# Kernel optimization log

Hardware: AMD Instinct MI355X
Metric: run time of the kernel (lower is better)

## Reference

```python
import jax, jax.numpy as jnp
import numpy as np

# ---- static config (aegnn GraphRes, ncars, spline convs) ----
B, NPG, DEG = 16, 6400, 8            # graphs per batch, nodes per graph, avg degree
N = B * NPG                          # 102400 nodes
E = N * DEG                          # 819200 edges
W_IMG, H_IMG = 120, 100              # input_shape[:2]
PSX, PSY = 16, 12                    # pooling_size
GX, GY = 8, 9                        # ceil(120/16), ceil(100/12)
G = GX * GY                          # 72 voxel-grid cells per graph
CH = [1, 8, 16, 16, 16, 32, 32, 32]  # n[] channel ladder, conv1..conv7
KK = 8                               # kernel_size**dim = 2**3 spline kernels
NUM_OUT = 2


def setup_inputs() -> dict:
    key = jax.random.key(0)
    ks = jax.random.split(key, 16)
    x = jax.random.normal(ks[0], (N, 1), jnp.float32)
    # event positions: (x,y,t) with x in [0,120), y in [0,100), t in [0,1)
    pos = jax.random.uniform(ks[1], (N, 3), jnp.float32) * jnp.array([W_IMG, H_IMG, 1.0], jnp.float32)
    # within-graph random edges
    eg = jax.random.randint(ks[2], (E,), 0, B)
    src = eg * NPG + jax.random.randint(ks[3], (E,), 0, NPG)
    dst = eg * NPG + jax.random.randint(ks[4], (E,), 0, NPG)
    edge_index = jnp.stack([src, dst]).astype(jnp.int32)
    # pseudo-coordinates (normalized relative positions) in [0,1]^3
    edge_attr = jax.random.uniform(ks[5], (E, 3), jnp.float32)
    batch = (jnp.arange(N) // NPG).astype(jnp.int32)
    params = {}
    for i in range(7):
        cin, cout = CH[i], CH[i + 1]
        params[f"w{i+1}"] = jax.random.normal(ks[6 + i], (KK, cin, cout), jnp.float32) / np.float32(np.sqrt(cin * KK))
    fc_w = jax.random.normal(ks[13], (G * CH[-1], NUM_OUT), jnp.float32) * 0.02
    return dict(x=x, pos=pos, edge_attr=edge_attr, edge_index=edge_index, batch=batch,
                fc_w=fc_w, **params)


def _spline_basis(edge_attr):
    """Degree-1 open B-spline basis, kernel_size=2 per dim -> dense [E, 8].
    With K=2: v = u*(K-1) = u, so per-dim basis is [1-u, u].
    Flattened kernel index = k0 + 2*k1 + 4*k2 (dim0 fastest, as in torch_spline_conv)."""
    u = jnp.clip(edge_attr, 0.0, 1.0)
    b = jnp.stack([1.0 - u, u], axis=-1)                      # [E, 3, 2]
    full = jnp.einsum('ea,eb,ec->ecba', b[:, 0], b[:, 1], b[:, 2])  # [E, k2, k1, k0]
    return full.reshape(-1, KK)


def _spline_conv(x, src, dst, basis, Wk):
    """SplineConv(bias=False, root_weight=False, aggr='mean')."""
    xj = x[src]                                               # gather [E, Cin]
    out = basis[:, 0:1] * (xj @ Wk[0])
    for k in range(1, KK):                                    # fixed 8 kernels
        out = out + basis[:, k:k + 1] * (xj @ Wk[k])
    agg = jax.ops.segment_sum(out, dst, num_segments=N)
    cnt = jax.ops.segment_sum(jnp.ones((src.shape[0], 1), x.dtype), dst, num_segments=N)
    return agg / jnp.maximum(cnt, 1.0)


def reference(x, pos, edge_attr, edge_index, batch, fc_w, w1, w2, w3, w4, w5, w6, w7):
    src, dst = edge_index[0], edge_index[1]
    basis = _spline_basis(edge_attr)                          # [E, 8]
    act = jax.nn.elu
    h = act(_spline_conv(x, src, dst, basis, w1))             # 1 -> 8
    h = act(_spline_conv(h, src, dst, basis, w2))             # 8 -> 16
    h_sc = h
    h = act(_spline_conv(h, src, dst, basis, w3))             # 16 -> 16
    h = act(_spline_conv(h, src, dst, basis, w4))             # 16 -> 16
    h = h + h_sc                                              # residual
    h = act(_spline_conv(h, src, dst, basis, w5))             # 16 -> 32
    h_sc = h
    h = act(_spline_conv(h, src, dst, basis, w6))             # 32 -> 32
    h = act(_spline_conv(h, src, dst, basis, w7))             # 32 -> 32
    h = h + h_sc                                              # residual
    # voxel-grid max pooling over (x, y) with cell size pooling_size
    cx = jnp.floor(pos[:, 0] / PSX).astype(jnp.int32)
    cy = jnp.floor(pos[:, 1] / PSY).astype(jnp.int32)
    cluster = batch * G + cy * GX + cx                        # [N]
    pooled = jax.ops.segment_max(h, cluster, num_segments=B * G)
    pooled = jnp.where(jnp.isfinite(pooled), pooled, 0.0)     # empty cells -> 0
    return pooled.reshape(B, G * CH[-1]) @ fc_w               # [B, num_outputs]
```

## Files before the change

kernel.cpp:

```cpp
#include <hip/hip_runtime.h>
#include <math.h>

namespace {
constexpr int N  = 102400;
constexpr int E  = 819200;
constexpr int B_ = 16;
constexpr int G  = 72;
constexpr int GX = 8;
constexpr int NB = N / 256;
constexpr int EB = E / 256;
}


__global__ __launch_bounds__(256) void count_kernel(const int* __restrict__ ei,
                                                    int* __restrict__ cnt) {
  int e = blockIdx.x * 256 + threadIdx.x;
  atomicAdd(&cnt[ei[E + e]], 1);
}

__global__ __launch_bounds__(256) void rcnt_kernel(const int* __restrict__ cnt,
                                                   float* __restrict__ rcnt) {
  int n = blockIdx.x * 256 + threadIdx.x;
  rcnt[n] = 1.0f / (float)max(cnt[n], 1);
}

__global__ __launch_bounds__(256) void reduce_cnt(const int* __restrict__ cnt,
                                                  int* __restrict__ bsum) {
  __shared__ int s[256];
  int i = blockIdx.x * 256 + threadIdx.x;
  s[threadIdx.x] = cnt[i];
  __syncthreads();
  for (int st = 128; st > 0; st >>= 1) {
    if (threadIdx.x < st) s[threadIdx.x] += s[threadIdx.x + st];
    __syncthreads();
  }
  if (threadIdx.x == 0) bsum[blockIdx.x] = s[0];
}

__global__ __launch_bounds__(512) void scan_bsum(const int* __restrict__ bsum,
                                                 int* __restrict__ boff) {
  __shared__ int s[512];
  int i = threadIdx.x;
  int v = (i < NB) ? bsum[i] : 0;
  s[i] = v;
  __syncthreads();
  for (int st = 1; st < 512; st <<= 1) {
    int t = (i >= st) ? s[i - st] : 0;
    __syncthreads();
    s[i] += t;
    __syncthreads();
  }
  if (i < NB) boff[i] = s[i] - v;
}

__global__ __launch_bounds__(256) void write_rowptr(const int* __restrict__ cnt,
                                                    const int* __restrict__ boff,
                                                    int* __restrict__ rowptr,
                                                    int* __restrict__ cursor) {
  __shared__ int s[256];
  int i = blockIdx.x * 256 + threadIdx.x;
  int v = cnt[i];
  s[threadIdx.x] = v;
  __syncthreads();
  for (int st = 1; st < 256; st <<= 1) {
    int t = (threadIdx.x >= st) ? s[threadIdx.x - st] : 0;
    __syncthreads();
    s[threadIdx.x] += t;
    __syncthreads();
  }
  int off = boff[blockIdx.x] + s[threadIdx.x] - v;
  rowptr[i] = off;
  cursor[i] = off;
  if (i == N - 1) rowptr[N] = off + v;
}

__global__ __launch_bounds__(256) void edge_scatter(const int* __restrict__ ei,
                                                    const float* __restrict__ ea,
                                                    int* __restrict__ cursor,
                                                    float4* __restrict__ rec) {
  int e = blockIdx.x * 256 + threadIdx.x;
  int src = ei[e];
  int dst = ei[E + e];
  float u0 = fminf(fmaxf(ea[3 * e + 0], 0.f), 1.f);
  float u1 = fminf(fmaxf(ea[3 * e + 1], 0.f), 1.f);
  float u2 = fminf(fmaxf(ea[3 * e + 2], 0.f), 1.f);
  int slot = atomicAdd(&cursor[dst], 1);
  rec[slot] = make_float4(__int_as_float(src), u0, u1, u2);
}


__global__ __launch_bounds__(256) void block_hist(const int* __restrict__ cnt,
                                                  int* __restrict__ bh) {
  __shared__ int h[64];
  if (threadIdx.x < 64) h[threadIdx.x] = 0;
  __syncthreads();
  int n = blockIdx.x * 256 + threadIdx.x;
  atomicAdd(&h[min(cnt[n], 63)], 1);
  __syncthreads();
  if (threadIdx.x < 64) bh[threadIdx.x * NB + blockIdx.x] = h[threadIdx.x];
}

__global__ __launch_bounds__(256) void scan_bh(int* __restrict__ bh) {
  constexpr int TOT = 64 * NB;
  constexpr int CH  = TOT / 256;
  __shared__ int part[256];
  const int t = threadIdx.x;
  const int base = t * CH;
  int s = 0;
  for (int i = 0; i < CH; i++) s += bh[base + i];
  part[t] = s;
  __syncthreads();
  for (int st = 1; st < 256; st <<= 1) {
    int v = (t >= st) ? part[t - st] : 0;
    __syncthreads();
    part[t] += v;
    __syncthreads();
  }
  int run = part[t] - s;
  for (int i = 0; i < CH; i++) {
    int v = bh[base + i];
    bh[base + i] = run;
    run += v;
  }
}

__global__ __launch_bounds__(256) void order_block(const int* __restrict__ cnt,
                                                   const int* __restrict__ bh,
                                                   const int* __restrict__ rowptr,
                                                   int* __restrict__ order,
                                                   int2* __restrict__ sdesc) {
  __shared__ int cur[64];
  if (threadIdx.x < 64) cur[threadIdx.x] = 0;
  __syncthreads();
  int n = blockIdx.x * 256 + threadIdx.x;
  int b = min(cnt[n], 63);
  int lr = atomicAdd(&cur[b], 1);
  int rb = rowptr[n], re = rowptr[n + 1];
  __syncthreads();
  if (threadIdx.x < 64) cur[threadIdx.x] = bh[threadIdx.x * NB + blockIdx.x];
  __syncthreads();
  int p = cur[b] + lr;
  order[p] = n;
  sdesc[p] = make_int2(rb, re);
}

__device__ __forceinline__ void atomicMaxFloat(float* addr, float val) {
  if (val >= 0.f)
    atomicMax(reinterpret_cast<int*>(addr), __float_as_int(val));
  else
    atomicMin(reinterpret_cast<unsigned int*>(addr), __float_as_uint(val));
}

template <int CIN, int COUT, bool RES, bool POOL>
__global__ __launch_bounds__(256, 4) void node_conv_v5(
    const float* __restrict__ X, const float* __restrict__ W,
    const float4* __restrict__ rec, const int2* __restrict__ sdesc,
    const int* __restrict__ order, const float* __restrict__ rcnt,
    const float* __restrict__ res, float* __restrict__ Y,
    const float* __restrict__ pos, const int* __restrict__ batch,
    float* __restrict__ pooled) {
  constexpr int TPN  = COUT / 4;
  constexpr int NPB  = 256 / TPN;
  constexpr int ROWF = (CIN >= 8) ? 8 * CIN : 12;

  __shared__ float sAgg[NPB * ROWF];

  const int tid  = threadIdx.x;
  const int wave = tid >> 6;
  const int lane = tid & 63;

  const int node_l = tid / TPN;
  const int co4 = tid % TPN;
  const int n2 = order[blockIdx.x * NPB + node_l];
  const float rc = rcnt[n2];
  float4 rres = make_float4(0.f, 0.f, 0.f, 0.f);
  if constexpr (RES)
    rres = *reinterpret_cast<const float4*>(res + (size_t)n2 * COUT + co4 * 4);
  float p0 = 0.f, p1 = 0.f;
  int bi = 0;
  if constexpr (POOL) {
    p0 = pos[n2 * 3 + 0];
    p1 = pos[n2 * 3 + 1];
    bi = batch[n2];
  }

  if constexpr (CIN >= 8) {
    constexpr int QN   = CIN / 4;
    constexpr int LPN  = 8 * QN;
    constexpr int NPW  = 64 / LPN;
    constexpr int REPS = NPB / (4 * NPW);

    const int ci4  = lane % QN;
    const int esub = (lane / QN) & 7;
    const int ns   = lane / LPN;
    const int kstar = ((lane / QN) & 1) * 4 + ((lane / (2 * QN)) & 1) * 2 +
                      ((lane / (4 * QN)) & 1);
    const int slot0 = wave * (REPS * NPW) + ns;

    auto loadDesc = [&](int rep) -> int2 {
      int r = min(rep, REPS - 1);
      return sdesc[blockIdx.x * NPB + slot0 + r * NPW];
    };
    auto loadRec = [&](int e) -> float4 { return rec[min(e, E - 1)]; };
    auto loadX = [&](const float4& r) -> float4 {
      int src = __float_as_int(r.x);
      return *(reinterpret_cast<const float4*>(X + (size_t)src * CIN) + ci4);
    };

    int2 d0 = loadDesc(0);
    int2 d1 = loadDesc(1);
    int2 d2 = loadDesc(2);
    float4 ra0 = loadRec(d0.x + esub), rb0 = loadRec(d0.x + esub + 8);
    float4 ra1 = loadRec(d1.x + esub), rb1 = loadRec(d1.x + esub + 8);
    float4 xa0 = loadX(ra0), xb0 = loadX(rb0);

#pragma unroll 1
    for (int rep = 0; rep < REPS; rep++) {
      float4 xa1 = loadX(ra1), xb1 = loadX(rb1);
      float4 ra2 = loadRec(d2.x + esub), rb2 = loadRec(d2.x + esub + 8);
      int2 d3 = loadDesc(rep + 3);

      float agg[32];
#pragma unroll
      for (int i = 0; i < 32; i++) agg[i] = 0.f;

      auto accum = [&](const float4& r, const float4& v, bool valid) {
        float uy = r.y, uz = r.z, uw = r.w;
        float py = 1.f - uy, pz = 1.f - uz, pw = 1.f - uw;
        float g = valid ? 1.f : 0.f;
        float t0 = py * pz * g, t1 = uy * pz * g;
        float t2 = py * uz * g, t3 = uy * uz * g;
        float b[8] = {t0 * pw, t1 * pw, t2 * pw, t3 * pw,
                      t0 * uw, t1 * uw, t2 * uw, t3 * uw};
#pragma unroll
        for (int k = 0; k < 8; k++) {
          agg[k * 4 + 0] = fmaf(b[k], v.x, agg[k * 4 + 0]);
          agg[k * 4 + 1] = fmaf(b[k], v.y, agg[k * 4 + 1]);
          agg[k * 4 + 2] = fmaf(b[k], v.z, agg[k * 4 + 2]);
          agg[k * 4 + 3] = fmaf(b[k], v.w, agg[k * 4 + 3]);
        }
      };

      accum(ra0, xa0, d0.x + esub < d0.y);
      accum(rb0, xb0, d0.x + esub + 8 < d0.y);
#pragma unroll 1
      for (int e = d0.x + esub + 16; e < d0.y; e += 8) {
        float4 rr = rec[e];
        float4 xx = loadX(rr);
        accum(rr, xx, true);
      }

#pragma unroll
      for (int s = 0; s < 3; s++) {
        const int m = QN << s;
        const int H = 16 >> s;
        bool up = (lane & m) != 0;
#pragma unroll
        for (int i = 0; i < H; i++) {
          float keep = up ? agg[i + H] : agg[i];
          float send = up ? agg[i] : agg[i + H];
          agg[i] = keep + __shfl_xor(send, m, 64);
        }
      }

      const int sl = slot0 + rep * NPW;
      const int idx4 = (kstar * QN + ci4) ^ (sl & 7);
      *reinterpret_cast<float4*>(&sAgg[sl * ROWF + idx4 * 4]) =
          make_float4(agg[0], agg[1], agg[2], agg[3]);

      d0 = d1; d1 = d2; d2 = d3;
      ra0 = ra1; rb0 = rb1; ra1 = ra2; rb1 = rb2;
      xa0 = xa1; xb0 = xb1;
    }
  } else {
    constexpr int LPN  = 8;
    constexpr int NPW  = 8;
    constexpr int REPS = NPB / (4 * NPW);
    const int ns = lane / LPN;
    const int k  = lane & 7;
    const int slotbase = blockIdx.x * NPB + wave * (REPS * NPW) + ns;

    int2 seC = sdesc[slotbase];
    int2 seN = (REPS > 1) ? sdesc[slotbase + NPW] : seC;
    float4 rcC = make_float4(0.f, 0.f, 0.f, 0.f);
    bool vC = seC.x < seC.y;
    if (vC) rcC = rec[seC.x];

#pragma unroll 1
    for (int rep = 0; rep < REPS; rep++) {
      bool vN = (rep + 1 < REPS) && (seN.x < seN.y);
      float4 rcN = make_float4(0.f, 0.f, 0.f, 0.f);
      if (vN) rcN = rec[seN.x];
      int2 seNN = (rep + 2 < REPS) ? sdesc[slotbase + (rep + 2) * NPW] : seN;

      float a0 = 0.f;
      if (vC) {
        float4 r = rcC;
        int e = seC.x + 1;
        while (true) {
          bool more = e < seC.y;
          float4 rn = r;
          if (more) rn = rec[e];
          int src = __float_as_int(r.x);
          float f0 = (k & 1) ? r.y : 1.f - r.y;
          float f1 = (k & 2) ? r.z : 1.f - r.z;
          float f2 = (k & 4) ? r.w : 1.f - r.w;
          a0 = fmaf(f0 * f1 * f2, X[src], a0);
          if (!more) break;
          r = rn;
          e++;
        }
      }

      const int sl = wave * (REPS * NPW) + rep * NPW + ns;
      sAgg[sl * ROWF + k] = a0;

      seC = seN;
      seN = seNN;
      vC = vN;
      rcC = rcN;
    }
  }
  __syncthreads();

  float4 acc = make_float4(0.f, 0.f, 0.f, 0.f);
  const float4* W4 = reinterpret_cast<const float4*>(W);
  const float* arow = &sAgg[node_l * ROWF];

  if constexpr (CIN == 1) {
#pragma unroll
    for (int kk = 0; kk < 8; kk++) {
      float a = arow[kk];
      float4 w = W4[kk * TPN + co4];
      acc.x = fmaf(a, w.x, acc.x);
      acc.y = fmaf(a, w.y, acc.y);
      acc.z = fmaf(a, w.z, acc.z);
      acc.w = fmaf(a, w.w, acc.w);
    }
  } else {
    constexpr int Q = CIN / 4;
    const int swz = node_l & 7;
#pragma unroll 2
    for (int kk = 0; kk < 8; kk++) {
#pragma unroll
      for (int c = 0; c < Q; c++) {
        float4 a4 = *reinterpret_cast<const float4*>(
            &arow[((kk * Q + c) ^ swz) * 4]);
        float4 w0 = W4[(kk * CIN + 4 * c + 0) * TPN + co4];
        float4 w1 = W4[(kk * CIN + 4 * c + 1) * TPN + co4];
        float4 w2 = W4[(kk * CIN + 4 * c + 2) * TPN + co4];
        float4 w3 = W4[(kk * CIN + 4 * c + 3) * TPN + co4];
        acc.x = fmaf(a4.x, w0.x, acc.x);
        acc.y = fmaf(a4.x, w0.y, acc.y);
        acc.z = fmaf(a4.x, w0.z, acc.z);
        acc.w = fmaf(a4.x, w0.w, acc.w);
        acc.x = fmaf(a4.y, w1.x, acc.x);
        acc.y = fmaf(a4.y, w1.y, acc.y);
        acc.z = fmaf(a4.y, w1.z, acc.z);
        acc.w = fmaf(a4.y, w1.w, acc.w);
        acc.x = fmaf(a4.z, w2.x, acc.x);
        acc.y = fmaf(a4.z, w2.y, acc.y);
        acc.z = fmaf(a4.z, w2.z, acc.z);
        acc.w = fmaf(a4.z, w2.w, acc.w);
        acc.x = fmaf(a4.w, w3.x, acc.x);
        acc.y = fmaf(a4.w, w3.y, acc.y);
        acc.z = fmaf(a4.w, w3.z, acc.z);
        acc.w = fmaf(a4.w, w3.w, acc.w);
      }
    }
  }

  float v[4] = {acc.x, acc.y, acc.z, acc.w};
#pragma unroll
  for (int i = 0; i < 4; i++) {
    float w = v[i] * rc;
    v[i] = w > 0.f ? w : expm1f(w);
  }
  if constexpr (RES) {
    v[0] += rres.x;
    v[1] += rres.y;
    v[2] += rres.z;
    v[3] += rres.w;
  }

  if constexpr (POOL) {
    int cx = (int)floorf(p0 / 16.0f);
    int cy = (int)floorf(p1 / 12.0f);
    int cl = bi * G + cy * GX + cx;
    float* pr = pooled + cl * 32 + co4 * 4;
#pragma unroll
    for (int i = 0; i < 4; i++) atomicMaxFloat(&pr[i], v[i]);
  } else {
    *reinterpret_cast<float4*>(Y + (size_t)n2 * COUT + co4 * 4) =
        make_float4(v[0], v[1], v[2], v[3]);
  }
}

__global__ __launch_bounds__(256) void fc_kernel(const float* __restrict__ pooled,
                                                 const float* __restrict__ fcw,
                                                 float* __restrict__ out) {
  int b = blockIdx.x >> 1;
  int o = blockIdx.x & 1;
  const float* pb = pooled + b * (G * 32);
  float s = 0.f;
  for (int i = threadIdx.x; i < G * 32; i += 256) {
    float v = pb[i];
    v = isfinite(v) ? v : 0.f;
    s += v * fcw[i * 2 + o];
  }
  __shared__ float red[256];
  red[threadIdx.x] = s;
  __syncthreads();
  for (int st = 128; st > 0; st >>= 1) {
    if (threadIdx.x < st) red[threadIdx.x] += red[threadIdx.x + st];
    __syncthreads();
  }
  if (threadIdx.x == 0) out[b * 2 + o] = red[0];
}

extern "C" void kernel_launch(void* const* d_in, const int* in_sizes, int n_in,
                              void* d_out, int out_size, void* d_ws, size_t ws_size,
                              hipStream_t stream) {
  const float* x     = (const float*)d_in[0];
  const float* pos   = (const float*)d_in[1];
  const float* ea    = (const float*)d_in[2];
  const int*   ei    = (const int*)d_in[3];
  const int*   batch = (const int*)d_in[4];
  const float* fcw   = (const float*)d_in[5];
  const float* w1    = (const float*)d_in[6];
  const float* w2    = (const float*)d_in[7];
  const float* w3    = (const float*)d_in[8];
  const float* w4    = (const float*)d_in[9];
  const float* w5    = (const float*)d_in[10];
  const float* w6    = (const float*)d_in[11];
  const float* w7    = (const float*)d_in[12];
  float* out = (float*)d_out;

  char* ws = (char*)d_ws;
  size_t off = 0;
  auto alloc = [&](size_t bytes) {
    size_t p = off;
    off += (bytes + 255) & ~(size_t)255;
    return ws + p;
  };
  float*  rcnt   = (float*)alloc((size_t)N * 4);
  int*    cnt    = (int*)alloc((size_t)N * 4);
  int*    rowptr = (int*)alloc((size_t)(N + 1) * 4);
  int*    cursor = (int*)alloc((size_t)N * 4);
  int*    bsum   = (int*)alloc(512 * 4);
  int*    boff   = (int*)alloc(512 * 4);
  int*    bh     = (int*)alloc((size_t)64 * NB * 4);
  int*    order  = (int*)alloc((size_t)N * 4);
  int2*   sdesc  = (int2*)alloc((size_t)N * 8);
  float4* rec    = (float4*)alloc((size_t)E * 16);
  float*  bufA   = (float*)alloc((size_t)N * 32 * 4);
  float*  bufB   = (float*)alloc((size_t)N * 32 * 4);
  float*  bufC   = (float*)alloc((size_t)N * 32 * 4);
  float*  pooled = (float*)alloc((size_t)B_ * G * 32 * 4);

  hipMemsetAsync(cnt, 0, (size_t)N * 4, stream);
  count_kernel<<<EB, 256, 0, stream>>>(ei, cnt);
  rcnt_kernel<<<NB, 256, 0, stream>>>(cnt, rcnt);
  reduce_cnt<<<NB, 256, 0, stream>>>(cnt, bsum);
  scan_bsum<<<1, 512, 0, stream>>>(bsum, boff);
  write_rowptr<<<NB, 256, 0, stream>>>(cnt, boff, rowptr, cursor);
  edge_scatter<<<EB, 256, 0, stream>>>(ei, ea, cursor, rec);

  block_hist<<<NB, 256, 0, stream>>>(cnt, bh);
  scan_bh<<<1, 256, 0, stream>>>(bh);
  order_block<<<NB, 256, 0, stream>>>(cnt, bh, rowptr, order, sdesc);

  hipMemsetAsync(pooled, 0xFF, (size_t)B_ * G * 32 * 4, stream);

  node_conv_v5<1, 8, false, false><<<N / 128, 256, 0, stream>>>(
      x, w1, rec, sdesc, order, rcnt, nullptr, bufA, nullptr, nullptr, nullptr);
  node_conv_v5<8, 16, false, false><<<N / 64, 256, 0, stream>>>(
      bufA, w2, rec, sdesc, order, rcnt, nullptr, bufB, nullptr, nullptr, nullptr);
  node_conv_v5<16, 16, false, false><<<N / 64, 256, 0, stream>>>(
      bufB, w3, rec, sdesc, order, rcnt, nullptr, bufC, nullptr, nullptr, nullptr);
  node_conv_v5<16, 16, true, false><<<N / 64, 256, 0, stream>>>(
      bufC, w4, rec, sdesc, order, rcnt, bufB, bufA, nullptr, nullptr, nullptr);
  node_conv_v5<16, 32, false, false><<<N / 32, 256, 0, stream>>>(
      bufA, w5, rec, sdesc, order, rcnt, nullptr, bufC, nullptr, nullptr, nullptr);
  node_conv_v5<32, 32, false, false><<<N / 32, 256, 0, stream>>>(
      bufC, w6, rec, sdesc, order, rcnt, nullptr, bufB, nullptr, nullptr, nullptr);
  node_conv_v5<32, 32, true, true><<<N / 32, 256, 0, stream>>>(
      bufB, w7, rec, sdesc, order, rcnt, bufC, nullptr, pos, batch, pooled);

  fc_kernel<<<B_ * 2, 256, 0, stream>>>(pooled, fcw, out);
}
```

Measured before the change: 698.9 us.

## Drop degree-sorted node ordering and swizzle block index across XCDs

Removes the degree-histogram bucketing pass (three kernels plus the order array) and processes nodes in natural order, writing the per-node edge range directly in the rowptr kernel. Conv kernels remap block indices so consecutive node chunks spread across the XCDs, and output and residual accesses become contiguous. This saves preprocessing launches and an indirection but gives up degree-balanced waves, so divergence from uneven edge counts may increase.

New measurement: 640.2 us (median of 2 runs). 8.4% less time.

```diff
diff --git a/kernel.cpp b/kernel.cpp
--- a/kernel.cpp
+++ b/kernel.cpp
@@ -56,7 +56,8 @@
 __global__ __launch_bounds__(256) void write_rowptr(const int* __restrict__ cnt,
                                                     const int* __restrict__ boff,
                                                     int* __restrict__ rowptr,
-                                                    int* __restrict__ cursor) {
+                                                    int* __restrict__ cursor,
+                                                    int2* __restrict__ sdesc) {
   __shared__ int s[256];
   int i = blockIdx.x * 256 + threadIdx.x;
   int v = cnt[i];
@@ -71,6 +72,7 @@
   int off = boff[blockIdx.x] + s[threadIdx.x] - v;
   rowptr[i] = off;
   cursor[i] = off;
+  sdesc[i] = make_int2(off, off + v);
   if (i == N - 1) rowptr[N] = off + v;
 }
 
@@ -88,62 +90,6 @@
   rec[slot] = make_float4(__int_as_float(src), u0, u1, u2);
 }
 
-
-__global__ __launch_bounds__(256) void block_hist(const int* __restrict__ cnt,
-                                                  int* __restrict__ bh) {
-  __shared__ int h[64];
-  if (threadIdx.x < 64) h[threadIdx.x] = 0;
-  __syncthreads();
-  int n = blockIdx.x * 256 + threadIdx.x;
-  atomicAdd(&h[min(cnt[n], 63)], 1);
-  __syncthreads();
-  if (threadIdx.x < 64) bh[threadIdx.x * NB + blockIdx.x] = h[threadIdx.x];
-}
-
-__global__ __launch_bounds__(256) void scan_bh(int* __restrict__ bh) {
-  constexpr int TOT = 64 * NB;
-  constexpr int CH  = TOT / 256;
-  __shared__ int part[256];
-  const int t = threadIdx.x;
-  const int base = t * CH;
-  int s = 0;
-  for (int i = 0; i < CH; i++) s += bh[base + i];
-  part[t] = s;
-  __syncthreads();
-  for (int st = 1; st < 256; st <<= 1) {
-    int v = (t >= st) ? part[t - st] : 0;
-    __syncthreads();
-    part[t] += v;
-    __syncthreads();
-  }
-  int run = part[t] - s;
-  for (int i = 0; i < CH; i++) {
-    int v = bh[base + i];
-    bh[base + i] = run;
-    run += v;
-  }
-}
-
-__global__ __launch_bounds__(256) void order_block(const int* __restrict__ cnt,
-                                                   const int* __restrict__ bh,
-                                                   const int* __restrict__ rowptr,
-                                                   int* __restrict__ order,
-                                                   int2* __restrict__ sdesc) {
-  __shared__ int cur[64];
-  if (threadIdx.x < 64) cur[threadIdx.x] = 0;
-  __syncthreads();
-  int n = blockIdx.x * 256 + threadIdx.x;
-  int b = min(cnt[n], 63);
-  int lr = atomicAdd(&cur[b], 1);
-  int rb = rowptr[n], re = rowptr[n + 1];
-  __syncthreads();
-  if (threadIdx.x < 64) cur[threadIdx.x] = bh[threadIdx.x * NB + blockIdx.x];
-  __syncthreads();
-  int p = cur[b] + lr;
-  order[p] = n;
-  sdesc[p] = make_int2(rb, re);
-}
-
 __device__ __forceinline__ void atomicMaxFloat(float* addr, float val) {
   if (val >= 0.f)
     atomicMax(reinterpret_cast<int*>(addr), __float_as_int(val));
@@ -152,13 +98,12 @@
 }
 
 template <int CIN, int COUT, bool RES, bool POOL>
-__global__ __launch_bounds__(256, 4) void node_conv_v5(
+__global__ __launch_bounds__(256, 4) void node_conv_v6(
     const float* __restrict__ X, const float* __restrict__ W,
     const float4* __restrict__ rec, const int2* __restrict__ sdesc,
-    const int* __restrict__ order, const float* __restrict__ rcnt,
-    const float* __restrict__ res, float* __restrict__ Y,
-    const float* __restrict__ pos, const int* __restrict__ batch,
-    float* __restrict__ pooled) {
+    const float* __restrict__ rcnt, const float* __restrict__ res,
+    float* __restrict__ Y, const float* __restrict__ pos,
+    const int* __restrict__ batch, float* __restrict__ pooled) {
   constexpr int TPN  = COUT / 4;
   constexpr int NPB  = 256 / TPN;
   constexpr int ROWF = (CIN >= 8) ? 8 * CIN : 12;
@@ -169,9 +114,12 @@
   const int wave = tid >> 6;
   const int lane = tid & 63;
 
+  const int sb = (blockIdx.x & 7) * (gridDim.x >> 3) + (blockIdx.x >> 3);
+  const int nbase = sb * NPB;
+
   const int node_l = tid / TPN;
   const int co4 = tid % TPN;
-  const int n2 = order[blockIdx.x * NPB + node_l];
+  const int n2 = nbase + node_l;
   const float rc = rcnt[n2];
   float4 rres = make_float4(0.f, 0.f, 0.f, 0.f);
   if constexpr (RES)
@@ -199,7 +147,7 @@
 
     auto loadDesc = [&](int rep) -> int2 {
       int r = min(rep, REPS - 1);
-      return sdesc[blockIdx.x * NPB + slot0 + r * NPW];
+      return sdesc[nbase + slot0 + r * NPW];
     };
     auto loadRec = [&](int e) -> float4 { return rec[min(e, E - 1)]; };
     auto loadX = [&](const float4& r) -> float4 {
@@ -278,7 +226,7 @@
     constexpr int REPS = NPB / (4 * NPW);
     const int ns = lane / LPN;
     const int k  = lane & 7;
-    const int slotbase = blockIdx.x * NPB + wave * (REPS * NPW) + ns;
+    const int slotbase = nbase + wave * (REPS * NPW) + ns;
 
     int2 seC = sdesc[slotbase];
     int2 seN = (REPS > 1) ? sdesc[slotbase + NPW] : seC;
@@ -449,8 +397,6 @@
   int*    cursor = (int*)alloc((size_t)N * 4);
   int*    bsum   = (int*)alloc(512 * 4);
   int*    boff   = (int*)alloc(512 * 4);
-  int*    bh     = (int*)alloc((size_t)64 * NB * 4);
-  int*    order  = (int*)alloc((size_t)N * 4);
   int2*   sdesc  = (int2*)alloc((size_t)N * 8);
   float4* rec    = (float4*)alloc((size_t)E * 16);
   float*  bufA   = (float*)alloc((size_t)N * 32 * 4);
@@ -463,29 +409,25 @@
   rcnt_kernel<<<NB, 256, 0, stream>>>(cnt, rcnt);
   reduce_cnt<<<NB, 256, 0, stream>>>(cnt, bsum);
   scan_bsum<<<1, 512, 0, stream>>>(bsum, boff);
-  write_rowptr<<<NB, 256, 0, stream>>>(cnt, boff, rowptr, cursor);
+  write_rowptr<<<NB, 256, 0, stream>>>(cnt, boff, rowptr, cursor, sdesc);
   edge_scatter<<<EB, 256, 0, stream>>>(ei, ea, cursor, rec);
 
-  block_hist<<<NB, 256, 0, stream>>>(cnt, bh);
-  scan_bh<<<1, 256, 0, stream>>>(bh);
-  order_block<<<NB, 256, 0, stream>>>(cnt, bh, rowptr, order, sdesc);
-
   hipMemsetAsync(pooled, 0xFF, (size_t)B_ * G * 32 * 4, stream);
 
-  node_conv_v5<1, 8, false, false><<<N / 128, 256, 0, stream>>>(
-      x, w1, rec, sdesc, order, rcnt, nullptr, bufA, nullptr, nullptr, nullptr);
-  node_conv_v5<8, 16, false, false><<<N / 64, 256, 0, stream>>>(
-      bufA, w2, rec, sdesc, order, rcnt, nullptr, bufB, nullptr, nullptr, nullptr);
-  node_conv_v5<16, 16, false, false><<<N / 64, 256, 0, stream>>>(
-      bufB, w3, rec, sdesc, order, rcnt, nullptr, bufC, nullptr, nullptr, nullptr);
-  node_conv_v5<16, 16, true, false><<<N / 64, 256, 0, stream>>>(
-      bufC, w4, rec, sdesc, order, rcnt, bufB, bufA, nullptr, nullptr, nullptr);
-  node_conv_v5<16, 32, false, false><<<N / 32, 256, 0, stream>>>(
-      bufA, w5, rec, sdesc, order, rcnt, nullptr, bufC, nullptr, nullptr, nullptr);
-  node_conv_v5<32, 32, false, false><<<N / 32, 256, 0, stream>>>(
-      bufC, w6, rec, sdesc, order, rcnt, nullptr, bufB, nullptr, nullptr, nullptr);
-  node_conv_v5<32, 32, true, true><<<N / 32, 256, 0, stream>>>(
-      bufB, w7, rec, sdesc, order, rcnt, bufC, nullptr, pos, batch, pooled);
+  node_conv_v6<1, 8, false, false><<<N / 128, 256, 0, stream>>>(
+      x, w1, rec, sdesc, rcnt, nullptr, bufA, nullptr, nullptr, nullptr);
+  node_conv_v6<8, 16, false, false><<<N / 64, 256, 0, stream>>>(
+      bufA, w2, rec, sdesc, rcnt, nullptr, bufB, nullptr, nullptr, nullptr);
+  node_conv_v6<16, 16, false, false><<<N / 64, 256, 0, stream>>>(
+      bufB, w3, rec, sdesc, rcnt, nullptr, bufC, nullptr, nullptr, nullptr);
+  node_conv_v6<16, 16, true, false><<<N / 64, 256, 0, stream>>>(
+      bufC, w4, rec, sdesc, rcnt, bufB, bufA, nullptr, nullptr, nullptr);
+  node_conv_v6<16, 32, false, false><<<N / 32, 256, 0, stream>>>(
+      bufA, w5, rec, sdesc, rcnt, nullptr, bufC, nullptr, nullptr, nullptr);
+  node_conv_v6<32, 32, false, false><<<N / 32, 256, 0, stream>>>(
+      bufC, w6, rec, sdesc, rcnt, nullptr, bufB, nullptr, nullptr, nullptr);
+  node_conv_v6<32, 32, true, true><<<N / 32, 256, 0, stream>>>(
+      bufB, w7, rec, sdesc, rcnt, bufC, nullptr, pos, batch, pooled);
 
   fc_kernel<<<B_ * 2, 256, 0, stream>>>(pooled, fcw, out);
 }
```
